# Optimization experiments

Hardware: AMD Instinct MI355X
Metric: run time of the kernel (lower is better)

## Reference

```python
import jax, jax.numpy as jnp
import numpy as np

# dims (match init_kwargs / input_specs)
D = 768      # embed_dim
H = 12       # num query heads
G = 4        # num kv groups
E = 8        # num experts
K = 2        # experts per token
F = 4 * D    # ffn hidden dim
B, S, T = 2, 1024, 1024
DH = D // H  # head dim = 64
EPS = 1e-6


def setup_inputs() -> dict:
    key = jax.random.key(0)
    ks = jax.random.split(key, 16)

    def p(k, shape, scale=0.02):
        return jax.random.normal(k, shape, jnp.float32) * scale

    inp = {}
    inp['x'] = jax.random.normal(ks[0], (B, S, D), jnp.float32)
    inp['encoder_context'] = jax.random.normal(ks[1], (B, T, D), jnp.float32)
    for n in ('ln1', 'ln2', 'ln3'):
        inp[n + '_scale'] = jnp.ones((D,), jnp.float32)
        inp[n + '_bias'] = jnp.zeros((D,), jnp.float32)
    i = 2
    for pre in ('sa', 'ca'):
        inp[pre + '_wq'] = p(ks[i], (D, H * DH)); i += 1
        inp[pre + '_bq'] = jnp.zeros((H * DH,), jnp.float32)
        inp[pre + '_wk'] = p(ks[i], (D, G * DH)); i += 1
        inp[pre + '_bk'] = jnp.zeros((G * DH,), jnp.float32)
        inp[pre + '_wv'] = p(ks[i], (D, G * DH)); i += 1
        inp[pre + '_bv'] = jnp.zeros((G * DH,), jnp.float32)
        inp[pre + '_wo'] = p(ks[i], (H * DH, D)); i += 1
        inp[pre + '_bo'] = jnp.zeros((D,), jnp.float32)
    inp['gate_w'] = p(ks[i], (D, E)); i += 1
    inp['gate_b'] = jnp.zeros((E,), jnp.float32)
    inp['w1'] = p(ks[i], (E, D, F)); i += 1
    inp['b1'] = jnp.zeros((E, F), jnp.float32)
    inp['w2'] = p(ks[i], (E, F, D)); i += 1
    inp['b2'] = jnp.zeros((E, D), jnp.float32)
    return inp


def _ln(x, scale, bias):
    mu = jnp.mean(x, axis=-1, keepdims=True)
    var = jnp.mean(jnp.square(x - mu), axis=-1, keepdims=True)
    return (x - mu) * jax.lax.rsqrt(var + EPS) * scale + bias


def _gqa(q_in, kv_in, wq, bq, wk, bk, wv, bv, wo, bo, causal):
    Bq, Sq, _ = q_in.shape
    Skv = kv_in.shape[1]
    q = (q_in @ wq + bq).reshape(Bq, Sq, H, DH)
    k = (kv_in @ wk + bk).reshape(Bq, Skv, G, DH)
    v = (kv_in @ wv + bv).reshape(Bq, Skv, G, DH)
    rep = H // G
    k = jnp.repeat(k, rep, axis=2)  # [B,Skv,H,DH]
    v = jnp.repeat(v, rep, axis=2)
    scores = jnp.einsum('bqhd,bkhd->bhqk', q, k) / jnp.sqrt(jnp.asarray(DH, q.dtype))
    if causal:
        cmask = jnp.tril(jnp.ones((Sq, Skv), bool))
        scores = jnp.where(cmask[None, None], scores, jnp.finfo(scores.dtype).min)
    attn = jax.nn.softmax(scores, axis=-1)
    out = jnp.einsum('bhqk,bkhd->bqhd', attn, v).reshape(Bq, Sq, H * DH)
    return out @ wo + bo


def _moe(x, gate_w, gate_b, w1, b1, w2, b2):
    logits = x @ gate_w + gate_b                      # [B,S,E]
    probs = jax.nn.softmax(logits, axis=-1)
    top_v, top_i = jax.lax.top_k(probs, K)            # [B,S,K]
    top_v = top_v / jnp.sum(top_v, axis=-1, keepdims=True)
    combine = jnp.sum(jax.nn.one_hot(top_i, E, dtype=x.dtype) * top_v[..., None], axis=-2)  # [B,S,E]
    h = jax.nn.gelu(jnp.einsum('bsd,edf->ebsf', x, w1) + b1[:, None, None, :])
    y = jnp.einsum('ebsf,efd->ebsd', h, w2) + b2[:, None, None, :]
    return jnp.einsum('ebsd,bse->bsd', y, combine)


def reference(x, encoder_context,
              ln1_scale, ln1_bias, ln2_scale, ln2_bias, ln3_scale, ln3_bias,
              sa_wq, sa_bq, sa_wk, sa_bk, sa_wv, sa_bv, sa_wo, sa_bo,
              ca_wq, ca_bq, ca_wk, ca_bk, ca_wv, ca_bv, ca_wo, ca_bo,
              gate_w, gate_b, w1, b1, w2, b2):
    xn = _ln(x, ln1_scale, ln1_bias)
    x = x + _gqa(xn, xn, sa_wq, sa_bq, sa_wk, sa_bk, sa_wv, sa_bv, sa_wo, sa_bo, causal=True)
    xn = _ln(x, ln2_scale, ln2_bias)
    x = x + _gqa(xn, encoder_context, ca_wq, ca_bq, ca_wk, ca_bk, ca_wv, ca_bv, ca_wo, ca_bo, causal=False)
    xn = _ln(x, ln3_scale, ln3_bias)
    x = x + _moe(xn, gate_w, gate_b, w1, b1, w2, b2)
    return x
```

## Files before the change

### kernel.cpp

```cpp
#include <hip/hip_runtime.h>

#define DEV __device__ __forceinline__

typedef __attribute__((ext_vector_type(4))) float f32x4;
typedef __attribute__((ext_vector_type(8))) short short8;
typedef __attribute__((ext_vector_type(4))) unsigned int u32x4;
typedef __attribute__((ext_vector_type(4))) unsigned short us16x4;

#define D_ 768
#define S_ 1024
#define B_ 2
#define H_ 12
#define G_ 4
#define DH_ 64
#define E_ 8
#define F_ 3072
#define NTOK (B_*S_)

#define GLDS16(g, l) __builtin_amdgcn_global_load_lds( \
    (const __attribute__((address_space(1))) void*)(g), \
    (__attribute__((address_space(3))) void*)(l), 16, 0, 0)

DEV unsigned short f2bf(float f){
  unsigned int b = __float_as_uint(f);
  b += 0x7FFFu + ((b >> 16) & 1u);
  return (unsigned short)(b >> 16);
}
DEV float bf2f(unsigned short h){ return __uint_as_float(((unsigned int)h) << 16); }
DEV unsigned int splitbf_pack(float v){
  unsigned short h = f2bf(v);
  unsigned short l = f2bf(v - bf2f(h));
  return (unsigned int)h | ((unsigned int)l << 16);
}

DEV short8 lds_swz(const unsigned short* base, int row, int chunk){
  return *(const short8*)((const char*)base + row*128 + (((chunk ^ (row & 7)) << 4)));
}
DEV short8 lds_swz32(const unsigned short* base, int row, int chunk){
  return *(const short8*)((const char*)base + row*64 + (((chunk ^ (row & 3)) << 4)));
}

DEV void swz_decode(int Fb, int nPanels, int& m, int& panel){
  int xcd = Fb & 7;
  int a = Fb >> 3;
  int mi = a & 3;
  int pid = (a >> 2)*8 + xcd;
  m = (pid / nPanels)*4 + mi;
  panel = pid % nPanels;
}

__global__ __launch_bounds__(256) void tcast_kernel(const float* __restrict__ W,
                                                    unsigned short* __restrict__ Wh,
                                                    unsigned short* __restrict__ Wl,
                                                    int K, int N){
  __shared__ float tile[32][33];
  long long zoff = (long long)blockIdx.z * K * N;
  const float* Wz = W + zoff;
  int n0 = blockIdx.x*32, k0 = blockIdx.y*32;
  int tx = threadIdx.x, ty = threadIdx.y;
  #pragma unroll
  for (int i=0;i<4;i++){
    int r = ty + i*8;
    tile[r][tx] = Wz[(long long)(k0+r)*N + n0 + tx];
  }
  __syncthreads();
  #pragma unroll
  for (int i=0;i<4;i++){
    int r = ty + i*8;
    float v = tile[tx][r];
    unsigned int hl = splitbf_pack(v);
    long long o = zoff + (long long)(n0+r)*K + k0 + tx;
    Wh[o] = (unsigned short)(hl & 0xFFFFu);
    if (Wl) Wl[o] = (unsigned short)(hl >> 16);
  }
}

__global__ void split_rows(const float* __restrict__ in, int ld, int width,
                           unsigned short* __restrict__ hi, unsigned short* __restrict__ lo){
  long long t = blockIdx.x;
  int c = threadIdx.x*4;
  f32x4 v = *(const f32x4*)(in + t*ld + c);
  unsigned int p0 = splitbf_pack(v.x), p1 = splitbf_pack(v.y);
  unsigned int p2 = splitbf_pack(v.z), p3 = splitbf_pack(v.w);
  us16x4 h, l;
  h.x=(unsigned short)p0; l.x=(unsigned short)(p0>>16);
  h.y=(unsigned short)p1; l.y=(unsigned short)(p1>>16);
  h.z=(unsigned short)p2; l.z=(unsigned short)(p2>>16);
  h.w=(unsigned short)p3; l.w=(unsigned short)(p3>>16);
  *(us16x4*)(hi + t*width + c) = h;
  *(us16x4*)(lo + t*width + c) = l;
}

__global__ void concat_bias(const float* __restrict__ b0, int n0,
                            const float* __restrict__ b1, int n1,
                            const float* __restrict__ b2, int n2,
                            float* __restrict__ out){
  int i = blockIdx.x*256 + threadIdx.x;
  if (i < n0) out[i] = b0[i];
  else if (i < n0+n1) out[i] = b1[i-n0];
  else if (i < n0+n1+n2) out[i] = b2[i-n0-n1];
}

__global__ __launch_bounds__(256) void ln_kernel(const float* __restrict__ x,
                                                 const float* __restrict__ sc,
                                                 const float* __restrict__ bi,
                                                 unsigned short* __restrict__ outh,
                                                 unsigned short* __restrict__ outl,
                                                 float* __restrict__ outf){
  __shared__ float red[8];
  long long row = blockIdx.x;
  const float* xr = x + row*D_;
  int tid = threadIdx.x;
  float v0 = xr[tid], v1 = xr[tid+256], v2 = xr[tid+512];
  float s = v0+v1+v2;
  float q = v0*v0 + v1*v1 + v2*v2;
  #pragma unroll
  for (int off=32; off; off>>=1){ s += __shfl_xor(s, off); q += __shfl_xor(q, off); }
  int lane = tid & 63, w = tid >> 6;
  if (lane == 0){ red[w] = s; red[4+w] = q; }
  __syncthreads();
  s = red[0]+red[1]+red[2]+red[3];
  q = red[4]+red[5]+red[6]+red[7];
  float mu  = s * (1.0f/D_);
  float var = q * (1.0f/D_) - mu*mu;
  float rstd = rsqrtf(var + 1e-6f);
  #pragma unroll
  for (int i=0;i<3;i++){
    int idx = tid + 256*i;
    float vv = (i==0) ? v0 : (i==1) ? v1 : v2;
    float o = (vv - mu)*rstd*sc[idx] + bi[idx];
    unsigned int pk = splitbf_pack(o);
    outh[row*D_ + idx] = (unsigned short)(pk & 0xFFFFu);
    if (outl) outl[row*D_ + idx] = (unsigned short)(pk >> 16);
    if (outf) outf[row*D_ + idx] = o;
  }
}

__global__ __launch_bounds__(256) void gemm3(
    int nX,
    const unsigned short* __restrict__ Ah, const unsigned short* __restrict__ Al, int lda,
    const unsigned short* __restrict__ Wh, const unsigned short* __restrict__ Wl, int K,
    const float* __restrict__ bias,
    const float* __restrict__ resid, int ldr,
    float* __restrict__ Cf, int ldc)
{
  __shared__ __align__(16) unsigned short AshH[128*64];
  __shared__ __align__(16) unsigned short AshL[128*64];
  __shared__ __align__(16) unsigned short BshH[64*64];
  __shared__ __align__(16) unsigned short BshL[64*64];
  int mB, panel;
  swz_decode(blockIdx.x, nX, mB, panel);
  const int r0 = mB*128;
  const int n0 = panel*64;
  const int tid = threadIdx.x;
  const int lane = tid & 63;
  const int wv = tid >> 6;
  const int wr = (wv>>1)*64, wc = (wv&1)*32;
  const int l15 = lane & 15, l4 = lane >> 4;
  const int sr = lane >> 3;
  const int sc = (lane & 7) ^ sr;

  f32x4 acc[4][2];
  #pragma unroll
  for (int i=0;i<4;i++)
    #pragma unroll
    for (int j=0;j<2;j++) acc[i][j] = (f32x4){0.f,0.f,0.f,0.f};

  for (int k0 = 0; k0 < K; k0 += 64){
    #pragma unroll
    for (int i=0;i<4;i++){
      int seg = wv*4 + i;
      long long src = (long long)(r0 + seg*8 + sr)*lda + k0 + sc*8;
      GLDS16(Ah + src, AshH + seg*8*64);
      GLDS16(Al + src, AshL + seg*8*64);
    }
    #pragma unroll
    for (int i=0;i<2;i++){
      int seg = wv*2 + i;
      long long src = (long long)(n0 + seg*8 + sr)*K + k0 + sc*8;
      GLDS16(Wh + src, BshH + seg*8*64);
      GLDS16(Wl + src, BshL + seg*8*64);
    }
    __syncthreads();
    #pragma unroll
    for (int ks=0; ks<2; ks++){
      int chunk = ks*4 + l4;
      short8 bh[2], bl[2];
      #pragma unroll
      for (int fj=0; fj<2; fj++){
        bh[fj] = lds_swz(BshH, wc + fj*16 + l15, chunk);
        bl[fj] = lds_swz(BshL, wc + fj*16 + l15, chunk);
      }
      #pragma unroll
      for (int fi=0; fi<4; fi++){
        short8 ah = lds_swz(AshH, wr + fi*16 + l15, chunk);
        short8 al = lds_swz(AshL, wr + fi*16 + l15, chunk);
        #pragma unroll
        for (int fj=0; fj<2; fj++){
          acc[fi][fj] = __builtin_amdgcn_mfma_f32_16x16x32_bf16(ah, bh[fj], acc[fi][fj], 0,0,0);
          acc[fi][fj] = __builtin_amdgcn_mfma_f32_16x16x32_bf16(al, bh[fj], acc[fi][fj], 0,0,0);
          acc[fi][fj] = __builtin_amdgcn_mfma_f32_16x16x32_bf16(ah, bl[fj], acc[fi][fj], 0,0,0);
        }
      }
    }
    __syncthreads();
  }

  #pragma unroll
  for (int fi=0; fi<4; fi++)
  #pragma unroll
  for (int fj=0; fj<2; fj++)
  #pragma unroll
  for (int reg=0; reg<4; reg++){
    int r = r0 + wr + fi*16 + l4*4 + reg;
    int col = n0 + wc + fj*16 + l15;
    float val = acc[fi][fj][reg] + bias[col];
    if (resid) val += resid[(long long)r*ldr + col];
    Cf[(long long)r*ldc + col] = val;
  }
}

__global__ __launch_bounds__(256) void gemm_nt128(
    int nX, int nzPerE,
    const unsigned short* __restrict__ A, int lda,
    const unsigned short* __restrict__ Wt, long long wstride,
    const float* __restrict__ bias, int bias_stride,
    const int* __restrict__ counts,
    const int* __restrict__ a_idx, int a_idx_stride,
    const int* __restrict__ row_base,
    float* __restrict__ Cf, long long partStride,
    unsigned short* __restrict__ Cb, int ldc,
    int K, int do_gelu)
{
  __shared__ __align__(16) unsigned short As[2][128*32];
  __shared__ __align__(16) unsigned short Bs[2][128*32];
  int mB, panel;
  swz_decode(blockIdx.x, nX*E_*nzPerE, mB, panel);
  const int n0 = (panel % nX)*128;
  const int zI = panel / nX;
  const int z = zI / nzPerE;
  const int kp = zI % nzPerE;
  const int Mz = counts[z];
  const int r0 = mB*128;
  if (r0 >= Mz) return;
  const int obase = row_base[z];
  const unsigned short* Wz = Wt + (long long)z*wstride;
  const float* bz = bias + (long long)z*bias_stride;
  const int kLen = K / nzPerE;
  const int kBeg = kp * kLen;
  const int tid = threadIdx.x;
  const int lane = tid & 63;
  const int wv = tid >> 6;
  const int wr = (wv>>1)*64, wc = (wv&1)*64;
  const int l15 = lane & 15, l4 = lane >> 4;
  const int r16 = lane >> 2;
  const int sc4 = (lane & 3) ^ (r16 & 3);

  long long arow[2];
  #pragma unroll
  for (int i=0;i<2;i++){
    int seg = wv*2 + i;
    int r = r0 + seg*16 + r16;
    int rcl = (r < Mz) ? r : (Mz-1);
    arow[i] = a_idx ? (long long)a_idx[(long long)z*a_idx_stride + rcl]
                    : (long long)(obase + rcl);
  }

  f32x4 acc[4][4];
  #pragma unroll
  for (int i=0;i<4;i++)
    #pragma unroll
    for (int j=0;j<4;j++) acc[i][j] = (f32x4){0.f,0.f,0.f,0.f};

  auto stage = [&](int buf, int k0){
    #pragma unroll
    for (int i=0;i<2;i++){
      int seg = wv*2 + i;
      GLDS16(A + arow[i]*lda + k0 + sc4*8, &As[buf][seg*512]);
      GLDS16(Wz + (long long)(n0 + seg*16 + r16)*K + k0 + sc4*8, &Bs[buf][seg*512]);
    }
  };

  const int nsteps = kLen >> 5;
  stage(0, kBeg);
  int cur = 0;
  for (int t=0; t<nsteps; t++){
    if (t+1 < nsteps){
      stage(cur^1, kBeg + (t+1)*32);
      asm volatile("s_waitcnt vmcnt(4)" ::: "memory");
    } else {
      asm volatile("s_waitcnt vmcnt(0)" ::: "memory");
    }
    __builtin_amdgcn_s_barrier();
    __builtin_amdgcn_sched_barrier(0);
    {
      short8 a[4], b[4];
      #pragma unroll
      for (int f=0; f<4; f++){
        a[f] = lds_swz32(&As[cur][0], wr + f*16 + l15, l4);
        b[f] = lds_swz32(&Bs[cur][0], wc + f*16 + l15, l4);
      }
      #pragma unroll
      for (int fi=0; fi<4; fi++)
        #pragma unroll
        for (int fj=0; fj<4; fj++)
          acc[fi][fj] = __builtin_amdgcn_mfma_f32_16x16x32_bf16(a[fi], b[fj], acc[fi][fj], 0,0,0);
    }
    __builtin_amdgcn_s_barrier();
    cur ^= 1;
  }

  #pragma unroll
  for (int fi=0; fi<4; fi++)
  #pragma unroll
  for (int fj=0; fj<4; fj++)
  #pragma unroll
  for (int reg=0; reg<4; reg++){
    int r = r0 + wr + fi*16 + l4*4 + reg;
    if (r >= Mz) continue;
    int col = n0 + wc + fj*16 + l15;
    float val = acc[fi][fj][reg] + (kp == 0 ? bz[col] : 0.0f);
    if (do_gelu){
      float xx = val;
      float u = 0.7978845608028654f*(xx + 0.044715f*xx*xx*xx);
      float t = 1.0f - 2.0f/(__expf(2.0f*u) + 1.0f);
      val = 0.5f*xx*(1.0f + t);
    }
    long long orow = (long long)obase + r;
    if (Cf) Cf[kp*partStride + orow*ldc + col] = val;
    if (Cb) Cb[orow*ldc + col] = f2bf(val);
  }
}

__global__ __launch_bounds__(256) void vt_split_kernel(const float* __restrict__ vin,
                                                       int ld, int cofs,
                                                       unsigned short* __restrict__ vth,
                                                       unsigned short* __restrict__ vtl){
  __shared__ float tile[32][33];
  int s0 = blockIdx.x*32, d0 = blockIdx.y*32;
  int bg = blockIdx.z; int b = bg >> 2, g = bg & 3;
  int tx = threadIdx.x, ty = threadIdx.y;
  #pragma unroll
  for (int i=0;i<4;i++){
    int r = ty + i*8;
    tile[r][tx] = vin[(long long)(b*1024 + s0 + r)*ld + cofs + g*64 + d0 + tx];
  }
  __syncthreads();
  #pragma unroll
  for (int i=0;i<4;i++){
    int d = d0 + ty + i*8;
    unsigned int pk = splitbf_pack(tile[tx][ty + i*8]);
    long long o = (long long)(bg*64 + d)*1024 + s0 + tx;
    vth[o] = (unsigned short)(pk & 0xFFFFu);
    vtl[o] = (unsigned short)(pk >> 16);
  }
}

#define AT_LDP 76
__global__ __launch_bounds__(256, 2) void attn_mfma(
    const float* __restrict__ q, int qld,
    const unsigned short* __restrict__ kh, const unsigned short* __restrict__ kl,
    const unsigned short* __restrict__ vth, const unsigned short* __restrict__ vtl,
    unsigned short* __restrict__ ctxh, unsigned short* __restrict__ ctxl, int causal)
{
  __shared__ __align__(16) unsigned short KhS[64*64];
  __shared__ __align__(16) unsigned short KlS[64*64];
  __shared__ __align__(16) unsigned short VhS[64*64];
  __shared__ __align__(16) unsigned short VlS[64*64];
  __shared__ __align__(16) unsigned int   Pp[4][16*AT_LDP];

  const int qblk = blockIdx.x;
  const int h = blockIdx.y;
  const int b = blockIdx.z;
  const int g = h / (H_/G_);
  const int tid = threadIdx.x;
  const int lane = tid & 63;
  const int w = tid >> 6;
  const int l15 = lane & 15;
  const int l4 = lane >> 4;
  const int sr = lane >> 3;
  const int sc = (lane & 7) ^ sr;
  const int qb0 = qblk*64;

  short8 qh[2], ql[2];
  #pragma unroll
  for (int ks=0; ks<2; ks++){
    const float* qp = q + ((long long)(b*S_ + qb0 + w*16 + l15))*qld + h*DH_ + ks*32 + l4*8;
    f32x4 q0 = *(const f32x4*)qp;
    f32x4 q1 = *(const f32x4*)(qp + 4);
    float qq[8] = {q0.x,q0.y,q0.z,q0.w,q1.x,q1.y,q1.z,q1.w};
    #pragma unroll
    for (int j=0;j<8;j++){
      unsigned int pk = splitbf_pack(qq[j]*0.125f);
      qh[ks][j] = (short)(pk & 0xFFFFu);
      ql[ks][j] = (short)(pk >> 16);
    }
  }

  f32x4 o[4];
  #pragma unroll
  for (int fd=0; fd<4; fd++) o[fd] = (f32x4){0.f,0.f,0.f,0.f};
  float m[4]    = {-3.0e38f,-3.0e38f,-3.0e38f,-3.0e38f};
  float lsum[4] = {0.f,0.f,0.f,0.f};

  const int ntiles = causal ? (qblk + 1) : (S_/64);
  for (int kt=0; kt<ntiles; kt++){
    __syncthreads();
    #pragma unroll
    for (int i=0;i<2;i++){
      int seg = w*2 + i;
      int row = seg*8 + sr;
      long long ksrc = (long long)(b*S_ + kt*64 + row)*(G_*DH_) + g*DH_ + sc*8;
      long long vsrc = (long long)((b*G_ + g)*64 + row)*S_ + kt*64 + sc*8;
      GLDS16(kh  + ksrc, KhS + seg*8*64);
      GLDS16(kl  + ksrc, KlS + seg*8*64);
      GLDS16(vth + vsrc, VhS + seg*8*64);
      GLDS16(vtl + vsrc, VlS + seg*8*64);
    }
    __syncthreads();

    f32x4 s[4];
    #pragma unroll
    for (int fj=0; fj<4; fj++) s[fj] = (f32x4){0.f,0.f,0.f,0.f};
    #pragma unroll
    for (int ks=0; ks<2; ks++){
      int chunk = ks*4 + l4;
      #pragma unroll
      for (int fj=0; fj<4; fj++){
        short8 bh = lds_swz(KhS, fj*16 + l15, chunk);
        short8 bl = lds_swz(KlS, fj*16 + l15, chunk);
        s[fj] = __builtin_amdgcn_mfma_f32_16x16x32_bf16(qh[ks], bh, s[fj], 0,0,0);
        s[fj] = __builtin_amdgcn_mfma_f32_16x16x32_bf16(ql[ks], bh, s[fj], 0,0,0);
        s[fj] = __builtin_amdgcn_mfma_f32_16x16x32_bf16(qh[ks], bl, s[fj], 0,0,0);
      }
    }

    if (causal && kt == qblk){
      #pragma unroll
      for (int fj=0; fj<4; fj++){
        int key = kt*64 + fj*16 + l15;
        #pragma unroll
        for (int reg=0; reg<4; reg++){
          int qr = qb0 + w*16 + l4*4 + reg;
          if (key > qr) s[fj][reg] = -3.0e38f;
        }
      }
    }

    float c[4], pmax[4];
    #pragma unroll
    for (int reg=0; reg<4; reg++){
      float mx = fmaxf(fmaxf(s[0][reg], s[1][reg]), fmaxf(s[2][reg], s[3][reg]));
      mx = fmaxf(mx, __shfl_xor(mx, 1));
      mx = fmaxf(mx, __shfl_xor(mx, 2));
      mx = fmaxf(mx, __shfl_xor(mx, 4));
      mx = fmaxf(mx, __shfl_xor(mx, 8));
      float mn = fmaxf(m[reg], mx);
      c[reg] = __expf(m[reg] - mn);
      m[reg] = mn;
      pmax[reg] = mn;
    }
    float psum[4] = {0.f,0.f,0.f,0.f};
    #pragma unroll
    for (int fj=0; fj<4; fj++){
      #pragma unroll
      for (int reg=0; reg<4; reg++){
        float pv = __expf(s[fj][reg] - pmax[reg]);
        psum[reg] += pv;
        Pp[w][(l4*4 + reg)*AT_LDP + fj*16 + l15] = splitbf_pack(pv);
      }
    }
    #pragma unroll
    for (int reg=0; reg<4; reg++){
      float ps = psum[reg];
      ps += __shfl_xor(ps, 1); ps += __shfl_xor(ps, 2);
      ps += __shfl_xor(ps, 4); ps += __shfl_xor(ps, 8);
      lsum[reg] = lsum[reg]*c[reg] + ps;
      o[0][reg] *= c[reg]; o[1][reg] *= c[reg];
      o[2][reg] *= c[reg]; o[3][reg] *= c[reg];
    }

    #pragma unroll
    for (int ks=0; ks<2; ks++){
      int chunk = ks*4 + l4;
      u32x4 pa = *(const u32x4*)&Pp[w][l15*AT_LDP + ks*32 + l4*8];
      u32x4 pb = *(const u32x4*)&Pp[w][l15*AT_LDP + ks*32 + l4*8 + 4];
      short8 ph, pl;
      #pragma unroll
      for (int j=0;j<4;j++){
        ph[j]   = (short)(pa[j] & 0xFFFFu); pl[j]   = (short)(pa[j] >> 16);
        ph[4+j] = (short)(pb[j] & 0xFFFFu); pl[4+j] = (short)(pb[j] >> 16);
      }
      #pragma unroll
      for (int fd=0; fd<4; fd++){
        short8 vh = lds_swz(VhS, fd*16 + l15, chunk);
        short8 vl = lds_swz(VlS, fd*16 + l15, chunk);
        o[fd] = __builtin_amdgcn_mfma_f32_16x16x32_bf16(ph, vh, o[fd], 0,0,0);
        o[fd] = __builtin_amdgcn_mfma_f32_16x16x32_bf16(pl, vh, o[fd], 0,0,0);
        o[fd] = __builtin_amdgcn_mfma_f32_16x16x32_bf16(ph, vl, o[fd], 0,0,0);
      }
    }
  }

  #pragma unroll
  for (int reg=0; reg<4; reg++){
    float inv = 1.0f / lsum[reg];
    long long tok = b*S_ + qb0 + w*16 + l4*4 + reg;
    #pragma unroll
    for (int fd=0; fd<4; fd++){
      unsigned int pk = splitbf_pack(o[fd][reg]*inv);
      long long oidx = tok*D_ + h*DH_ + fd*16 + l15;
      ctxh[oidx] = (unsigned short)(pk & 0xFFFFu);
      ctxl[oidx] = (unsigned short)(pk >> 16);
    }
  }
}

__global__ __launch_bounds__(256) void gate_kernel(const float* __restrict__ xnf,
                                                   const float* __restrict__ gw,
                                                   const float* __restrict__ gb,
                                                   int* __restrict__ counts,
                                                   int* __restrict__ toklist,
                                                   int* __restrict__ route_e,
                                                   int* __restrict__ route_pos,
                                                   float* __restrict__ route_w){
  int t = blockIdx.x*4 + (threadIdx.x >> 6);
  int lane = threadIdx.x & 63;
  float acc[E_];
  #pragma unroll
  for (int e=0;e<E_;e++) acc[e] = 0.f;
  #pragma unroll
  for (int i=0;i<12;i++){
    int d = lane + 64*i;
    float xv = xnf[(long long)t*D_ + d];
    const float* w = gw + (long long)d*E_;
    #pragma unroll
    for (int e=0;e<E_;e++) acc[e] += xv*w[e];
  }
  #pragma unroll
  for (int off=32; off; off>>=1)
    #pragma unroll
    for (int e=0;e<E_;e++) acc[e] += __shfl_xor(acc[e], off);
  if (lane == 0){
    #pragma unroll
    for (int e=0;e<E_;e++) acc[e] += gb[e];
    int e0 = 0;
    #pragma unroll
    for (int e=1;e<E_;e++) if (acc[e] > acc[e0]) e0 = e;
    int e1 = -1;
    #pragma unroll
    for (int e=0;e<E_;e++) if (e != e0 && (e1 < 0 || acc[e] > acc[e1])) e1 = e;
    float w0 = 1.0f/(1.0f + __expf(acc[e1] - acc[e0]));
    float w1 = 1.0f - w0;
    int p0 = atomicAdd(&counts[e0], 1);
    int p1 = atomicAdd(&counts[e1], 1);
    toklist[e0*NTOK + p0] = t;
    toklist[e1*NTOK + p1] = t;
    route_e[2*t]   = e0; route_e[2*t+1]   = e1;
    route_pos[2*t] = p0; route_pos[2*t+1] = p1;
    route_w[2*t]   = w0; route_w[2*t+1]   = w1;
  }
}

__global__ void offsets_kernel(const int* __restrict__ counts, int* __restrict__ offs){
  if (threadIdx.x == 0){
    int s = 0;
    for (int e=0;e<E_;e++){ offs[e] = s; s += counts[e]; }
  }
}

__global__ __launch_bounds__(192) void combine_kernel(const float* __restrict__ xb,
                                                      const float* __restrict__ y,
                                                      long long partStride,
                                                      const int* __restrict__ route_e,
                                                      const int* __restrict__ route_pos,
                                                      const float* __restrict__ route_w,
                                                      const int* __restrict__ offs,
                                                      float* __restrict__ out){
  int t = blockIdx.x;
  int i = threadIdx.x;
  int e0 = route_e[2*t], e1 = route_e[2*t+1];
  long long s0 = offs[e0] + route_pos[2*t];
  long long s1 = offs[e1] + route_pos[2*t+1];
  float w0 = route_w[2*t], w1 = route_w[2*t+1];
  f32x4 xv = *(const f32x4*)(xb + (long long)t*D_ + i*4);
  f32x4 y0 = (f32x4){0.f,0.f,0.f,0.f};
  f32x4 y1 = (f32x4){0.f,0.f,0.f,0.f};
  #pragma unroll
  for (int kp=0; kp<4; kp++){
    y0 += *(const f32x4*)(y + kp*partStride + s0*D_ + i*4);
    y1 += *(const f32x4*)(y + kp*partStride + s1*D_ + i*4);
  }
  f32x4 o = xv + w0*y0 + w1*y1;
  *(f32x4*)(out + (long long)t*D_ + i*4) = o;
}

extern "C" void kernel_launch(void* const* d_in, const int* in_sizes, int n_in,
                              void* d_out, int out_size, void* d_ws, size_t ws_size,
                              hipStream_t stream) {
  (void)in_sizes; (void)n_in; (void)out_size; (void)ws_size;
  const float* x     = (const float*)d_in[0];
  const float* enc   = (const float*)d_in[1];
  const float* ln1s  = (const float*)d_in[2];
  const float* ln1b  = (const float*)d_in[3];
  const float* ln2s  = (const float*)d_in[4];
  const float* ln2b  = (const float*)d_in[5];
  const float* ln3s  = (const float*)d_in[6];
  const float* ln3b  = (const float*)d_in[7];
  const float* sa_wq = (const float*)d_in[8];
  const float* sa_bq = (const float*)d_in[9];
  const float* sa_wk = (const float*)d_in[10];
  const float* sa_bk = (const float*)d_in[11];
  const float* sa_wv = (const float*)d_in[12];
  const float* sa_bv = (const float*)d_in[13];
  const float* sa_wo = (const float*)d_in[14];
  const float* sa_bo = (const float*)d_in[15];
  const float* ca_wq = (const float*)d_in[16];
  const float* ca_bq = (const float*)d_in[17];
  const float* ca_wk = (const float*)d_in[18];
  const float* ca_bk = (const float*)d_in[19];
  const float* ca_wv = (const float*)d_in[20];
  const float* ca_bv = (const float*)d_in[21];
  const float* ca_wo = (const float*)d_in[22];
  const float* ca_bo = (const float*)d_in[23];
  const float* gate_w= (const float*)d_in[24];
  const float* gate_b= (const float*)d_in[25];
  const float* w1    = (const float*)d_in[26];
  const float* b1    = (const float*)d_in[27];
  const float* w2    = (const float*)d_in[28];
  const float* b2    = (const float*)d_in[29];
  float* out = (float*)d_out;

  char* p = (char*)d_ws;
  auto alloc = [&](size_t bytes)->void*{
    void* r = (void*)p;
    p += (bytes + 255) & ~(size_t)255;
    return r;
  };
  unsigned short* wqkvh_sa = (unsigned short*)alloc((size_t)1280*768*2);
  unsigned short* wqkvl_sa = (unsigned short*)alloc((size_t)1280*768*2);
  unsigned short* woh_sa   = (unsigned short*)alloc((size_t)768*768*2);
  unsigned short* wol_sa   = (unsigned short*)alloc((size_t)768*768*2);
  unsigned short* wqh_ca   = (unsigned short*)alloc((size_t)768*768*2);
  unsigned short* wql_ca   = (unsigned short*)alloc((size_t)768*768*2);
  unsigned short* wkvh_ca  = (unsigned short*)alloc((size_t)512*768*2);
  unsigned short* wkvl_ca  = (unsigned short*)alloc((size_t)512*768*2);
  unsigned short* woh_ca   = (unsigned short*)alloc((size_t)768*768*2);
  unsigned short* wol_ca   = (unsigned short*)alloc((size_t)768*768*2);
  unsigned short* w1T = (unsigned short*)alloc((size_t)E_*D_*F_*2);
  unsigned short* w2T = (unsigned short*)alloc((size_t)E_*D_*F_*2);
  float* bqkv_sa = (float*)alloc(1280*4);
  float* bkv_ca  = (float*)alloc(512*4);
  unsigned short* ench = (unsigned short*)alloc((size_t)NTOK*D_*2);
  unsigned short* encl = (unsigned short*)alloc((size_t)NTOK*D_*2);
  unsigned short* xh   = (unsigned short*)alloc((size_t)NTOK*D_*2);
  unsigned short* xl   = (unsigned short*)alloc((size_t)NTOK*D_*2);
  unsigned short* ctxh = (unsigned short*)alloc((size_t)NTOK*D_*2);
  unsigned short* ctxl = (unsigned short*)alloc((size_t)NTOK*D_*2);
  unsigned short* xn_b = (unsigned short*)alloc((size_t)NTOK*D_*2);
  unsigned short* hbuf = (unsigned short*)alloc((size_t)2*NTOK*F_*2);
  unsigned short* khp   = (unsigned short*)alloc((size_t)NTOK*G_*DH_*2);
  unsigned short* klp   = (unsigned short*)alloc((size_t)NTOK*G_*DH_*2);
  unsigned short* vtp_h = (unsigned short*)alloc((size_t)NTOK*G_*DH_*2);
  unsigned short* vtp_l = (unsigned short*)alloc((size_t)NTOK*G_*DH_*2);
  float* qkvbuf = (float*)alloc((size_t)NTOK*1280*4);
  float* xnf  = (float*)alloc((size_t)NTOK*D_*4);
  float* xbuf = (float*)alloc((size_t)NTOK*D_*4);
  float* ybuf = (float*)alloc((size_t)8*NTOK*D_*4);
  int* counts    = (int*)alloc(E_*4);
  int* offs      = (int*)alloc(E_*4);
  int* toklist   = (int*)alloc((size_t)E_*NTOK*4);
  int* route_e   = (int*)alloc((size_t)2*NTOK*4);
  int* route_pos = (int*)alloc((size_t)2*NTOK*4);
  float* route_w = (float*)alloc((size_t)2*NTOK*4);

  (void)hipMemsetAsync(counts, 0, E_*sizeof(int), stream);

  dim3 tb(32,8);
  tcast_kernel<<<dim3(24,24,1), tb, 0, stream>>>(sa_wq, wqkvh_sa,            wqkvl_sa,            768, 768);
  tcast_kernel<<<dim3( 8,24,1), tb, 0, stream>>>(sa_wk, wqkvh_sa + 768*768,  wqkvl_sa + 768*768,  768, 256);
  tcast_kernel<<<dim3( 8,24,1), tb, 0, stream>>>(sa_wv, wqkvh_sa + 1024*768, wqkvl_sa + 1024*768, 768, 256);
  tcast_kernel<<<dim3(24,24,1), tb, 0, stream>>>(sa_wo, woh_sa, wol_sa, 768, 768);
  tcast_kernel<<<dim3(24,24,1), tb, 0, stream>>>(ca_wq, wqh_ca, wql_ca, 768, 768);
  tcast_kernel<<<dim3( 8,24,1), tb, 0, stream>>>(ca_wk, wkvh_ca,           wkvl_ca,           768, 256);
  tcast_kernel<<<dim3( 8,24,1), tb, 0, stream>>>(ca_wv, wkvh_ca + 256*768, wkvl_ca + 256*768, 768, 256);
  tcast_kernel<<<dim3(24,24,1), tb, 0, stream>>>(ca_wo, woh_ca, wol_ca, 768, 768);
  tcast_kernel<<<dim3(96,24,E_), tb, 0, stream>>>(w1, w1T, nullptr, 768, 3072);
  tcast_kernel<<<dim3(24,96,E_), tb, 0, stream>>>(w2, w2T, nullptr, 3072, 768);
  concat_bias<<<5, 256, 0, stream>>>(sa_bq, 768, sa_bk, 256, sa_bv, 256, bqkv_sa);
  concat_bias<<<2, 256, 0, stream>>>(ca_bk, 256, ca_bv, 256, nullptr, 0, bkv_ca);
  split_rows<<<NTOK, 192, 0, stream>>>(enc, 768, 768, ench, encl);

  ln_kernel<<<NTOK, 256, 0, stream>>>(x, ln1s, ln1b, xh, xl, nullptr);
  gemm3<<<20*16, 256, 0, stream>>>(20, xh, xl, 768, wqkvh_sa, wqkvl_sa, 768,
      bqkv_sa, nullptr, 0, qkvbuf, 1280);
  split_rows<<<NTOK, 64, 0, stream>>>(qkvbuf + 768, 1280, 256, khp, klp);
  vt_split_kernel<<<dim3(32,2,8), tb, 0, stream>>>(qkvbuf, 1280, 1024, vtp_h, vtp_l);
  attn_mfma<<<dim3(16,12,2), 256, 0, stream>>>(qkvbuf, 1280, khp, klp, vtp_h, vtp_l, ctxh, ctxl, 1);
  gemm3<<<12*16, 256, 0, stream>>>(12, ctxh, ctxl, 768, woh_sa, wol_sa, 768,
      sa_bo, x, 768, xbuf, 768);

  ln_kernel<<<NTOK, 256, 0, stream>>>(xbuf, ln2s, ln2b, xh, xl, nullptr);
  gemm3<<<12*16, 256, 0, stream>>>(12, xh, xl, 768, wqh_ca, wql_ca, 768,
      ca_bq, nullptr, 0, qkvbuf, 1280);
  gemm3<<<8*16, 256, 0, stream>>>(8, ench, encl, 768, wkvh_ca, wkvl_ca, 768,
      bkv_ca, nullptr, 0, qkvbuf + 768, 1280);
  split_rows<<<NTOK, 64, 0, stream>>>(qkvbuf + 768, 1280, 256, khp, klp);
  vt_split_kernel<<<dim3(32,2,8), tb, 0, stream>>>(qkvbuf, 1280, 1024, vtp_h, vtp_l);
  attn_mfma<<<dim3(16,12,2), 256, 0, stream>>>(qkvbuf, 1280, khp, klp, vtp_h, vtp_l, ctxh, ctxl, 0);
  gemm3<<<12*16, 256, 0, stream>>>(12, ctxh, ctxl, 768, woh_ca, wol_ca, 768,
      ca_bo, xbuf, 768, xbuf, 768);

  ln_kernel<<<NTOK, 256, 0, stream>>>(xbuf, ln3s, ln3b, xn_b, nullptr, xnf);
  gate_kernel<<<NTOK/4, 256, 0, stream>>>(xnf, gate_w, gate_b,
      counts, toklist, route_e, route_pos, route_w);
  offsets_kernel<<<1, 64, 0, stream>>>(counts, offs);
  gemm_nt128<<<24*16*E_, 256, 0, stream>>>(24, 1, xn_b, 768, w1T, (long long)F_*D_, b1, F_,
      counts, toklist, NTOK, offs, nullptr, 0, hbuf, F_, 768, 1);
  long long partStride = (long long)2*NTOK*D_;
  gemm_nt128<<<6*16*E_*4, 256, 0, stream>>>(6, 4, hbuf, F_, w2T, (long long)F_*D_, b2, D_,
      counts, nullptr, 0, offs, ybuf, partStride, nullptr, 768, F_, 0);
  combine_kernel<<<NTOK, 192, 0, stream>>>(xbuf, ybuf, partStride,
      route_e, route_pos, route_w, offs, out);
}
```

Baseline: 515.7 us.

## Double-buffer gemm3 K-loop and triple-buffer MoE grouped GEMM loads

gemm3 (split-bf16 three-MFMA GEMM) moves from a single-buffered 64-wide K step with full syncthreads to a double-buffered 32-wide K pipeline. The next tile's global-to-LDS loads are issued before computing the current one, and partial vmcnt waits are used. The MoE grouped GEMM goes from two to three LDS buffers with a prefetch distance of two steps, to hide more global load latency. The trade-off is more LDS per block, which may reduce occupancy, and gemm3 now does twice as many barrier iterations.

```diff
diff --git a/kernel.cpp b/kernel.cpp
--- a/kernel.cpp
+++ b/kernel.cpp
@@ -144,10 +144,10 @@
     const float* __restrict__ resid, int ldr,
     float* __restrict__ Cf, int ldc)
 {
-  __shared__ __align__(16) unsigned short AshH[128*64];
-  __shared__ __align__(16) unsigned short AshL[128*64];
-  __shared__ __align__(16) unsigned short BshH[64*64];
-  __shared__ __align__(16) unsigned short BshL[64*64];
+  __shared__ __align__(16) unsigned short AshH[2][128*32];
+  __shared__ __align__(16) unsigned short AshL[2][128*32];
+  __shared__ __align__(16) unsigned short BshH[2][64*32];
+  __shared__ __align__(16) unsigned short BshL[2][64*32];
   int mB, panel;
   swz_decode(blockIdx.x, nX, mB, panel);
   const int r0 = mB*128;
@@ -157,8 +157,8 @@
   const int wv = tid >> 6;
   const int wr = (wv>>1)*64, wc = (wv&1)*32;
   const int l15 = lane & 15, l4 = lane >> 4;
-  const int sr = lane >> 3;
-  const int sc = (lane & 7) ^ sr;
+  const int r16 = lane >> 2;
+  const int sc4 = (lane & 3) ^ (r16 & 3);
 
   f32x4 acc[4][2];
   #pragma unroll
@@ -166,35 +166,45 @@
     #pragma unroll
     for (int j=0;j<2;j++) acc[i][j] = (f32x4){0.f,0.f,0.f,0.f};
 
-  for (int k0 = 0; k0 < K; k0 += 64){
-    #pragma unroll
-    for (int i=0;i<4;i++){
-      int seg = wv*4 + i;
-      long long src = (long long)(r0 + seg*8 + sr)*lda + k0 + sc*8;
-      GLDS16(Ah + src, AshH + seg*8*64);
-      GLDS16(Al + src, AshL + seg*8*64);
-    }
+  auto stage = [&](int buf, int k0){
     #pragma unroll
     for (int i=0;i<2;i++){
       int seg = wv*2 + i;
-      long long src = (long long)(n0 + seg*8 + sr)*K + k0 + sc*8;
-      GLDS16(Wh + src, BshH + seg*8*64);
-      GLDS16(Wl + src, BshL + seg*8*64);
-    }
-    __syncthreads();
-    #pragma unroll
-    for (int ks=0; ks<2; ks++){
-      int chunk = ks*4 + l4;
+      long long src = (long long)(r0 + seg*16 + r16)*lda + k0 + sc4*8;
+      GLDS16(Ah + src, &AshH[buf][seg*512]);
+      GLDS16(Al + src, &AshL[buf][seg*512]);
+    }
+    {
+      int seg = wv;
+      long long src = (long long)(n0 + seg*16 + r16)*K + k0 + sc4*8;
+      GLDS16(Wh + src, &BshH[buf][seg*512]);
+      GLDS16(Wl + src, &BshL[buf][seg*512]);
+    }
+  };
+
+  const int nsteps = K >> 5;
+  stage(0, 0);
+  int cur = 0;
+  for (int t=0; t<nsteps; t++){
+    if (t+1 < nsteps){
+      stage(cur^1, (t+1)*32);
+      asm volatile("s_waitcnt vmcnt(6)" ::: "memory");
+    } else {
+      asm volatile("s_waitcnt vmcnt(0)" ::: "memory");
+    }
+    __builtin_amdgcn_s_barrier();
+    __builtin_amdgcn_sched_barrier(0);
+    {
       short8 bh[2], bl[2];
       #pragma unroll
       for (int fj=0; fj<2; fj++){
-        bh[fj] = lds_swz(BshH, wc + fj*16 + l15, chunk);
-        bl[fj] = lds_swz(BshL, wc + fj*16 + l15, chunk);
+        bh[fj] = lds_swz32(&BshH[cur][0], wc + fj*16 + l15, l4);
+        bl[fj] = lds_swz32(&BshL[cur][0], wc + fj*16 + l15, l4);
       }
       #pragma unroll
       for (int fi=0; fi<4; fi++){
-        short8 ah = lds_swz(AshH, wr + fi*16 + l15, chunk);
-        short8 al = lds_swz(AshL, wr + fi*16 + l15, chunk);
+        short8 ah = lds_swz32(&AshH[cur][0], wr + fi*16 + l15, l4);
+        short8 al = lds_swz32(&AshL[cur][0], wr + fi*16 + l15, l4);
         #pragma unroll
         for (int fj=0; fj<2; fj++){
           acc[fi][fj] = __builtin_amdgcn_mfma_f32_16x16x32_bf16(ah, bh[fj], acc[fi][fj], 0,0,0);
@@ -203,7 +213,8 @@
         }
       }
     }
-    __syncthreads();
+    __builtin_amdgcn_s_barrier();
+    cur ^= 1;
   }
 
   #pragma unroll
@@ -232,8 +243,8 @@
     unsigned short* __restrict__ Cb, int ldc,
     int K, int do_gelu)
 {
-  __shared__ __align__(16) unsigned short As[2][128*32];
-  __shared__ __align__(16) unsigned short Bs[2][128*32];
+  __shared__ __align__(16) unsigned short As[3][128*32];
+  __shared__ __align__(16) unsigned short Bs[3][128*32];
   int mB, panel;
   swz_decode(blockIdx.x, nX*E_*nzPerE, mB, panel);
   const int n0 = (panel % nX)*128;
@@ -283,10 +294,14 @@
 
   const int nsteps = kLen >> 5;
   stage(0, kBeg);
+  if (nsteps > 1) stage(1, kBeg + 32);
   int cur = 0;
   for (int t=0; t<nsteps; t++){
-    if (t+1 < nsteps){
-      stage(cur^1, kBeg + (t+1)*32);
+    if (t+2 < nsteps){
+      int nb = cur + 2; if (nb >= 3) nb -= 3;
+      stage(nb, kBeg + (t+2)*32);
+      asm volatile("s_waitcnt vmcnt(8)" ::: "memory");
+    } else if (t+1 < nsteps){
       asm volatile("s_waitcnt vmcnt(4)" ::: "memory");
     } else {
       asm volatile("s_waitcnt vmcnt(0)" ::: "memory");
@@ -307,7 +322,7 @@
           acc[fi][fj] = __builtin_amdgcn_mfma_f32_16x16x32_bf16(a[fi], b[fj], acc[fi][fj], 0,0,0);
     }
     __builtin_amdgcn_s_barrier();
-    cur ^= 1;
+    cur += 1; if (cur >= 3) cur = 0;
   }
 
   #pragma unroll
```

Measured after the change: 533.7 us. 1.03x slower.
